# Kernel optimization log

Measured on AMD Instinct MI355X. Metric: run time of the kernel, lower is better.

## Reference

```python
import jax, jax.numpy as jnp
import numpy as np

N, E, B = 100000, 1000000, 64
DIN, DS, H, NG = 128, 1024, 256, 20


def setup_inputs() -> dict:
    key = jax.random.key(0)
    ks = jax.random.split(key, 48)
    lin = lambda k, i, o: (jax.random.normal(k, (i, o), jnp.float32) / np.sqrt(i)).astype(jnp.float32)
    inp = {
        'x': jax.random.normal(ks[0], (N, DIN), jnp.float32),
        'edge_index': jax.random.randint(ks[1], (2, E), 0, N, jnp.int32),
        'batch': jnp.sort(jax.random.randint(ks[2], (N,), 0, B, jnp.int32)),
        'static_features': jax.random.normal(ks[3], (B, DS), jnp.float32),
        'temporal_feats': jax.random.normal(ks[4], (B, 5), jnp.float32),
        'type_idx': jax.random.randint(ks[5], (B,), 0, 10, jnp.int32),
        'type_emb': jax.random.normal(ks[6], (10, H), jnp.float32),
        # static encoder
        'Ws1': lin(ks[7], DS, H), 'bs1': jnp.zeros(H), 'Ws2': lin(ks[8], H, H), 'bs2': jnp.zeros(H),
        # 3 GCN convs
        'Wc1': lin(ks[9], DIN, H), 'bc1': jnp.zeros(H),
        'Wc2': lin(ks[10], H, H), 'bc2': jnp.zeros(H),
        'Wc3': lin(ks[11], H, H), 'bc3': jnp.zeros(H),
        # residual dim_match linears
        'Wd1': lin(ks[12], DIN, H), 'bd1': jnp.zeros(H),
        'Wd2': lin(ks[13], H, H), 'bd2': jnp.zeros(H),
        'Wd3': lin(ks[14], H, H), 'bd3': jnp.zeros(H),
        # temporal MLP (5 -> H//2 -> H)
        'Wt1': lin(ks[15], 5, H // 2), 'bt1': jnp.zeros(H // 2),
        'Wt2': lin(ks[16], H // 2, H), 'bt2': jnp.zeros(H),
        # pattern detector
        'Wp1': lin(ks[17], H, H // 2), 'bp1': jnp.zeros(H // 2),
        'Wp2': lin(ks[18], H // 2, H), 'bp2': jnp.zeros(H),
        # fusion (5H -> 2H -> H)
        'Wf1': lin(ks[19], 5 * H, 2 * H), 'bf1': jnp.zeros(2 * H),
        'Wf2': lin(ks[20], 2 * H, H), 'bf2': jnp.zeros(H),
        # heads
        'Wg': lin(ks[21], H, NG), 'bg': jnp.zeros(NG),
        'Wtp': lin(ks[22], H, 1), 'btp': jnp.zeros(1),
    }
    return inp


def reference(x, edge_index, batch, static_features, temporal_feats, type_idx, type_emb,
              Ws1, bs1, Ws2, bs2,
              Wc1, bc1, Wc2, bc2, Wc3, bc3,
              Wd1, bd1, Wd2, bd2, Wd3, bd3,
              Wt1, bt1, Wt2, bt2,
              Wp1, bp1, Wp2, bp2,
              Wf1, bf1, Wf2, bf2,
              Wg, bg, Wtp, btp):
    n = x.shape[0]
    b = static_features.shape[0]
    src, dst = edge_index[0], edge_index[1]
    # GCN symmetric norm with self-loops: deg = 1 + in-degree
    deg = 1.0 + jax.ops.segment_sum(jnp.ones(src.shape[0], x.dtype), dst, num_segments=n)
    dinv = deg ** -0.5
    ew = dinv[src] * dinv[dst]  # [E] edge norm weights

    def gcn(h_in, W, bias):
        h = h_in @ W  # [n, H]
        agg = jax.ops.segment_sum(h[src] * ew[:, None], dst, num_segments=n)
        return agg + h / deg[:, None] + bias  # neighbor agg + self-loop + bias

    # 3 GCN layers with residual dim_match (dropout is identity at inference)
    x1 = jax.nn.relu(gcn(x, Wc1, bc1)) + (x @ Wd1 + bd1)
    x2 = jax.nn.relu(gcn(x1, Wc2, bc2)) + (x1 @ Wd2 + bd2)
    x3 = jax.nn.relu(gcn(x2, Wc3, bc3)) + (x2 @ Wd3 + bd3)

    pat = jax.nn.relu(jax.nn.relu(x3 @ Wp1 + bp1) @ Wp2 + bp2)

    counts = jnp.maximum(jax.ops.segment_sum(jnp.ones(n, x.dtype), batch, num_segments=b), 1.0)
    graph_embed = jax.ops.segment_sum(x3, batch, num_segments=b) / counts[:, None]
    pattern_embed = jax.ops.segment_sum(pat, batch, num_segments=b) / counts[:, None]

    static_embed = jax.nn.relu(static_features @ Ws1 + bs1) @ Ws2 + bs2
    temporal_embed = jax.nn.relu(temporal_feats @ Wt1 + bt1) @ Wt2 + bt2
    type_embed = type_emb[type_idx]

    combined = jnp.concatenate([graph_embed, static_embed, temporal_embed, type_embed, pattern_embed], axis=1)
    fused = jax.nn.relu(combined @ Wf1 + bf1) @ Wf2 + bf2
    group_logits = fused @ Wg + bg
    time_pred = fused @ Wtp + btp
    return fused, group_logits, time_pred
```

## Files before the change

kernel.cpp:

```cpp
#include <hip/hip_runtime.h>

#define H 256
#define LDK 40

typedef __attribute__((ext_vector_type(8))) short bf16x8;
typedef __attribute__((ext_vector_type(4))) float f32x4;

__device__ __forceinline__ float b2f(ushort h) {
    return __uint_as_float(((unsigned)h) << 16);
}
__device__ __forceinline__ ushort f2bf(float f) {
    unsigned u = __float_as_uint(f);
    unsigned r = (u + 0x7FFF + ((u >> 16) & 1)) >> 16;
    return (ushort)r;
}

__global__ __launch_bounds__(256) void k_zero_i(int* p, int n) {
    int i = blockIdx.x * 256 + threadIdx.x;
    if (i < n) p[i] = 0;
}

__global__ __launch_bounds__(256) void k_zero_f(float* p, int n) {
    int i = blockIdx.x * 256 + threadIdx.x;
    if (i < n) p[i] = 0.f;
}

__global__ __launch_bounds__(256) void k_count_deg_i(const int* __restrict__ dst, int* cnt, int E) {
    int i = blockIdx.x * 256 + threadIdx.x;
    if (i < E) atomicAdd(&cnt[dst[i]], 1);
}

__global__ __launch_bounds__(256) void k_scan1(const int* __restrict__ cnt, int* __restrict__ partial,
                                               int* __restrict__ bsums, int N) {
    __shared__ int s[256];
    int t = threadIdx.x;
    int idx = blockIdx.x * 256 + t;
    int v = idx < N ? cnt[idx] : 0;
    s[t] = v;
    __syncthreads();
    for (int off = 1; off < 256; off <<= 1) {
        int add = (t >= off) ? s[t - off] : 0;
        __syncthreads();
        s[t] += add;
        __syncthreads();
    }
    if (idx < N) partial[idx] = s[t];
    if (t == 255) bsums[blockIdx.x] = s[t];
}

__global__ __launch_bounds__(1024) void k_scan2(int* bsums, int nb) {
    __shared__ int s[1024];
    int t = threadIdx.x;
    s[t] = (t < nb) ? bsums[t] : 0;
    __syncthreads();
    for (int off = 1; off < 1024; off <<= 1) {
        int add = (t >= off) ? s[t - off] : 0;
        __syncthreads();
        s[t] += add;
        __syncthreads();
    }
    if (t < nb) bsums[t] = s[t];
}

__global__ __launch_bounds__(256) void k_scan3(const int* __restrict__ partial, const int* __restrict__ bsums,
                                               int* __restrict__ rowptr, int N) {
    int idx = blockIdx.x * 256 + threadIdx.x;
    if (idx < N) {
        int off = blockIdx.x > 0 ? bsums[blockIdx.x - 1] : 0;
        rowptr[idx + 1] = partial[idx] + off;
        if (idx == 0) rowptr[0] = 0;
    }
}

__global__ __launch_bounds__(256) void k_finish_deg_i(const int* __restrict__ cnt,
                                                      float* __restrict__ dinv,
                                                      float* __restrict__ selfw, int N) {
    int i = blockIdx.x * 256 + threadIdx.x;
    if (i < N) {
        float d = 1.0f + (float)cnt[i];
        dinv[i] = rsqrtf(d);
        selfw[i] = 1.0f / d;
    }
}

__global__ __launch_bounds__(256) void k_scatter(const int* __restrict__ src, const int* __restrict__ dst,
                                                 const float* __restrict__ dinv, const int* __restrict__ rowptr,
                                                 int* __restrict__ fill, int* __restrict__ esrc,
                                                 float* __restrict__ ewt, int E) {
    int e = blockIdx.x * 256 + threadIdx.x;
    if (e >= E) return;
    int s = src[e], d = dst[e];
    int pos = rowptr[d] + atomicAdd(&fill[d], 1);
    esrc[pos] = s;
    ewt[pos] = dinv[s] * dinv[d];
}

__global__ __launch_bounds__(256) void k_cvt(const float* __restrict__ in, ushort* __restrict__ out, long n) {
    long i = (long)blockIdx.x * 256 + threadIdx.x;
    if (i < n) out[i] = f2bf(in[i]);
}

__global__ __launch_bounds__(256) void k_tcvt(const float* __restrict__ W, ushort* __restrict__ Wt,
                                              int K, int M) {
    int idx = blockIdx.x * 256 + threadIdx.x;
    if (idx >= K * M) return;
    int k = idx / M, m = idx - k * M;
    Wt[(size_t)m * K + k] = f2bf(W[idx]);
}

__global__ __launch_bounds__(256) void k_gather_b4(const ushort* __restrict__ xin, const int* __restrict__ rowptr,
                                                   const int* __restrict__ esrc, const float* __restrict__ ewt,
                                                   const float* __restrict__ selfw, ushort* __restrict__ p,
                                                   int N, int SX, int SP) {
    int node = blockIdx.x * 4 + (threadIdx.x >> 6);
    if (node >= N) return;
    int c = (threadIdx.x & 63) << 2;
    ushort4 h = *(const ushort4*)(xin + (size_t)node * SX + c);
    float sw = selfw[node];
    float a0 = b2f(h.x) * sw, a1 = b2f(h.y) * sw, a2 = b2f(h.z) * sw, a3 = b2f(h.w) * sw;
    int j = rowptr[node], r1 = rowptr[node + 1];
    for (; j + 3 < r1; j += 4) {
        int s0 = esrc[j], s1 = esrc[j + 1], s2 = esrc[j + 2], s3 = esrc[j + 3];
        float w0 = ewt[j], w1 = ewt[j + 1], w2 = ewt[j + 2], w3 = ewt[j + 3];
        ushort4 v0 = *(const ushort4*)(xin + (size_t)s0 * SX + c);
        ushort4 v1 = *(const ushort4*)(xin + (size_t)s1 * SX + c);
        ushort4 v2 = *(const ushort4*)(xin + (size_t)s2 * SX + c);
        ushort4 v3 = *(const ushort4*)(xin + (size_t)s3 * SX + c);
        a0 += b2f(v0.x) * w0 + b2f(v1.x) * w1 + b2f(v2.x) * w2 + b2f(v3.x) * w3;
        a1 += b2f(v0.y) * w0 + b2f(v1.y) * w1 + b2f(v2.y) * w2 + b2f(v3.y) * w3;
        a2 += b2f(v0.z) * w0 + b2f(v1.z) * w1 + b2f(v2.z) * w2 + b2f(v3.z) * w3;
        a3 += b2f(v0.w) * w0 + b2f(v1.w) * w1 + b2f(v2.w) * w2 + b2f(v3.w) * w3;
    }
    for (; j < r1; ++j) {
        int s0 = esrc[j];
        float w0 = ewt[j];
        ushort4 v0 = *(const ushort4*)(xin + (size_t)s0 * SX + c);
        a0 += b2f(v0.x) * w0; a1 += b2f(v0.y) * w0; a2 += b2f(v0.z) * w0; a3 += b2f(v0.w) * w0;
    }
    ushort4 o;
    o.x = f2bf(a0); o.y = f2bf(a1); o.z = f2bf(a2); o.w = f2bf(a3);
    *(ushort4*)(p + (size_t)node * SP + c) = o;
}

__global__ __launch_bounds__(256) void k_gather_b2(const ushort* __restrict__ xin, const int* __restrict__ rowptr,
                                                   const int* __restrict__ esrc, const float* __restrict__ ewt,
                                                   const float* __restrict__ selfw, ushort* __restrict__ p,
                                                   int N, int SX, int SP) {
    int node = blockIdx.x * 4 + (threadIdx.x >> 6);
    if (node >= N) return;
    int c = (threadIdx.x & 63) << 1;
    ushort2 h = *(const ushort2*)(xin + (size_t)node * SX + c);
    float sw = selfw[node];
    float a0 = b2f(h.x) * sw, a1 = b2f(h.y) * sw;
    int j = rowptr[node], r1 = rowptr[node + 1];
    for (; j + 3 < r1; j += 4) {
        int s0 = esrc[j], s1 = esrc[j + 1], s2 = esrc[j + 2], s3 = esrc[j + 3];
        float w0 = ewt[j], w1 = ewt[j + 1], w2 = ewt[j + 2], w3 = ewt[j + 3];
        ushort2 v0 = *(const ushort2*)(xin + (size_t)s0 * SX + c);
        ushort2 v1 = *(const ushort2*)(xin + (size_t)s1 * SX + c);
        ushort2 v2 = *(const ushort2*)(xin + (size_t)s2 * SX + c);
        ushort2 v3 = *(const ushort2*)(xin + (size_t)s3 * SX + c);
        a0 += b2f(v0.x) * w0 + b2f(v1.x) * w1 + b2f(v2.x) * w2 + b2f(v3.x) * w3;
        a1 += b2f(v0.y) * w0 + b2f(v1.y) * w1 + b2f(v2.y) * w2 + b2f(v3.y) * w3;
    }
    for (; j < r1; ++j) {
        int s0 = esrc[j];
        float w0 = ewt[j];
        ushort2 v0 = *(const ushort2*)(xin + (size_t)s0 * SX + c);
        a0 += b2f(v0.x) * w0; a1 += b2f(v0.y) * w0;
    }
    ushort2 o;
    o.x = f2bf(a0); o.y = f2bf(a1);
    *(ushort2*)(p + (size_t)node * SP + c) = o;
}

__global__ __launch_bounds__(256, 2) void k_fused_mfma(
    const ushort* __restrict__ Pm, const ushort* __restrict__ X,
    const ushort* __restrict__ Wct, const ushort* __restrict__ Wdt,
    const float* __restrict__ bc, const float* __restrict__ bd,
    ushort* __restrict__ Out, int N, int K, int SP, int SX) {
    __shared__ short Ps[64 * LDK];
    __shared__ short Xs[64 * LDK];
    __shared__ short Wcs[256 * LDK];
    __shared__ short Wds[256 * LDK];
    const int tid = threadIdx.x;
    const int wave = tid >> 6, lane = tid & 63;
    const int row0 = blockIdx.x * 64;

    f32x4 accC[4][4], accD[4][4];
#pragma unroll
    for (int i = 0; i < 4; ++i)
#pragma unroll
        for (int j = 0; j < 4; ++j) { accC[i][j] = (f32x4)0.f; accD[i][j] = (f32x4)0.f; }

    const int sr = tid >> 2, sc = (tid & 3) * 8;
    int grow = row0 + sr; if (grow > N - 1) grow = N - 1;
    const int m = lane & 15, kh = (lane >> 4) * 8;

    for (int k0 = 0; k0 < K; k0 += 32) {
        *(uint4*)&Ps[sr * LDK + sc] = *(const uint4*)(Pm + (size_t)grow * SP + k0 + sc);
        *(uint4*)&Xs[sr * LDK + sc] = *(const uint4*)(X + (size_t)grow * SX + k0 + sc);
#pragma unroll
        for (int p = 0; p < 4; ++p) {
            int col = p * 64 + (tid >> 2);
            *(uint4*)&Wcs[col * LDK + sc] = *(const uint4*)(Wct + (size_t)col * K + k0 + sc);
            *(uint4*)&Wds[col * LDK + sc] = *(const uint4*)(Wdt + (size_t)col * K + k0 + sc);
        }
        __syncthreads();
        bf16x8 aP[4], aX[4], bC[4], bD[4];
#pragma unroll
        for (int i = 0; i < 4; ++i) {
            aP[i] = *(bf16x8*)&Ps[(16 * i + m) * LDK + kh];
            aX[i] = *(bf16x8*)&Xs[(16 * i + m) * LDK + kh];
        }
#pragma unroll
        for (int j = 0; j < 4; ++j) {
            int c = wave * 64 + 16 * j + m;
            bC[j] = *(bf16x8*)&Wcs[c * LDK + kh];
            bD[j] = *(bf16x8*)&Wds[c * LDK + kh];
        }
#pragma unroll
        for (int i = 0; i < 4; ++i)
#pragma unroll
            for (int j = 0; j < 4; ++j) {
                accC[i][j] = __builtin_amdgcn_mfma_f32_16x16x32_bf16(aP[i], bC[j], accC[i][j], 0, 0, 0);
                accD[i][j] = __builtin_amdgcn_mfma_f32_16x16x32_bf16(aX[i], bD[j], accD[i][j], 0, 0, 0);
            }
        __syncthreads();
    }

    const int rq = (lane >> 4) * 4;
#pragma unroll
    for (int j = 0; j < 4; ++j) {
        int col = wave * 64 + 16 * j + m;
        float bcv = bc[col], bdv = bd[col];
#pragma unroll
        for (int i = 0; i < 4; ++i)
#pragma unroll
            for (int g = 0; g < 4; ++g) {
                int row = row0 + 16 * i + rq + g;
                if (row < N) {
                    float v = fmaxf(accC[i][j][g] + bcv, 0.f) + accD[i][j][g] + bdv;
                    Out[(size_t)row * 256 + col] = f2bf(v);
                }
            }
    }
}

__global__ __launch_bounds__(256, 2) void k_gemm_mfma(
    const ushort* __restrict__ A, const ushort* __restrict__ Wt, const float* __restrict__ bias,
    ushort* __restrict__ Out, int N, int K, int M, int SA, int dorelu) {
    __shared__ short As[128 * LDK];
    __shared__ short Wls[256 * LDK];
    const int tid = threadIdx.x;
    const int wave = tid >> 6, lane = tid & 63;
    const int MW = M >> 6;
    const int R = 16384 / M;
    const int row0 = blockIdx.x * R;
    const int row_off = (wave / MW) * 64, col_off = (wave % MW) * 64;

    f32x4 acc[4][4];
#pragma unroll
    for (int i = 0; i < 4; ++i)
#pragma unroll
        for (int j = 0; j < 4; ++j) acc[i][j] = (f32x4)0.f;

    const int m = lane & 15, kh = (lane >> 4) * 8, sc = (tid & 3) * 8;

    for (int k0 = 0; k0 < K; k0 += 32) {
        for (int c = tid; c < R * 4; c += 256) {
            int r = c >> 2, ck = (c & 3) * 8;
            int gr = row0 + r; if (gr > N - 1) gr = N - 1;
            *(uint4*)&As[r * LDK + ck] = *(const uint4*)(A + (size_t)gr * SA + k0 + ck);
        }
        for (int p = 0; p < MW; ++p) {
            int col = p * 64 + (tid >> 2);
            *(uint4*)&Wls[col * LDK + sc] = *(const uint4*)(Wt + (size_t)col * K + k0 + sc);
        }
        __syncthreads();
        bf16x8 af[4], bf[4];
#pragma unroll
        for (int i = 0; i < 4; ++i) af[i] = *(bf16x8*)&As[(row_off + 16 * i + m) * LDK + kh];
#pragma unroll
        for (int j = 0; j < 4; ++j) bf[j] = *(bf16x8*)&Wls[(col_off + 16 * j + m) * LDK + kh];
#pragma unroll
        for (int i = 0; i < 4; ++i)
#pragma unroll
            for (int j = 0; j < 4; ++j)
                acc[i][j] = __builtin_amdgcn_mfma_f32_16x16x32_bf16(af[i], bf[j], acc[i][j], 0, 0, 0);
        __syncthreads();
    }

    const int rq = (lane >> 4) * 4;
#pragma unroll
    for (int j = 0; j < 4; ++j) {
        int col = col_off + 16 * j + m;
        float bv = bias[col];
#pragma unroll
        for (int i = 0; i < 4; ++i)
#pragma unroll
            for (int g = 0; g < 4; ++g) {
                int row = row0 + row_off + 16 * i + rq + g;
                if (row < N) {
                    float v = acc[i][j][g] + bv;
                    if (dorelu) v = fmaxf(v, 0.f);
                    Out[(size_t)row * M + col] = f2bf(v);
                }
            }
    }
}

__global__ __launch_bounds__(256, 2) void k_pat2_pool(
    const ushort* __restrict__ A, const ushort* __restrict__ Wt, const float* __restrict__ bias,
    const int* __restrict__ batch, float* __restrict__ pesum, int N, int K, int SA) {
    __shared__ short As[64 * LDK];
    __shared__ short Wls[256 * LDK];
    __shared__ int sbatch[64];
    const int tid = threadIdx.x;
    const int wave = tid >> 6, lane = tid & 63;
    const int row0 = blockIdx.x * 64;
    const int col_off = wave * 64;

    f32x4 acc[4][4];
#pragma unroll
    for (int i = 0; i < 4; ++i)
#pragma unroll
        for (int j = 0; j < 4; ++j) acc[i][j] = (f32x4)0.f;

    const int m = lane & 15, kh = (lane >> 4) * 8, sc = (tid & 3) * 8;
    if (tid < 64) {
        int r = row0 + tid;
        sbatch[tid] = batch[r < N ? r : (N - 1)];
    }

    for (int k0 = 0; k0 < K; k0 += 32) {
        {
            int r = tid >> 2, ck = (tid & 3) * 8;
            int gr = row0 + r; if (gr > N - 1) gr = N - 1;
            *(uint4*)&As[r * LDK + ck] = *(const uint4*)(A + (size_t)gr * SA + k0 + ck);
        }
#pragma unroll
        for (int p = 0; p < 4; ++p) {
            int col = p * 64 + (tid >> 2);
            *(uint4*)&Wls[col * LDK + sc] = *(const uint4*)(Wt + (size_t)col * K + k0 + sc);
        }
        __syncthreads();
        bf16x8 af[4], bf[4];
#pragma unroll
        for (int i = 0; i < 4; ++i) af[i] = *(bf16x8*)&As[(16 * i + m) * LDK + kh];
#pragma unroll
        for (int j = 0; j < 4; ++j) bf[j] = *(bf16x8*)&Wls[(col_off + 16 * j + m) * LDK + kh];
#pragma unroll
        for (int i = 0; i < 4; ++i)
#pragma unroll
            for (int j = 0; j < 4; ++j)
                acc[i][j] = __builtin_amdgcn_mfma_f32_16x16x32_bf16(af[i], bf[j], acc[i][j], 0, 0, 0);
        __syncthreads();
    }

    const int rq = (lane >> 4) * 4;
    const int g0 = sbatch[0];
    const int g1 = sbatch[63];
    for (int g = g0; g <= g1; ++g) {
#pragma unroll
        for (int j = 0; j < 4; ++j) {
            float bv = bias[col_off + 16 * j + m];
            float s = 0.f;
#pragma unroll
            for (int i = 0; i < 4; ++i)
#pragma unroll
                for (int q = 0; q < 4; ++q) {
                    int rl = 16 * i + rq + q;
                    bool ok = (sbatch[rl] == g) && (row0 + rl < N);
                    float v = fmaxf(acc[i][j][q] + bv, 0.f);
                    s += ok ? v : 0.f;
                }
            s += __shfl_down(s, 32, 64);
            s += __shfl_down(s, 16, 64);
            if (lane < 16) atomicAdd(&pesum[(size_t)g * 256 + col_off + 16 * j + lane], s);
        }
    }
}

__global__ void k_ranges(const int* __restrict__ batch, int N, int B, int* __restrict__ start,
                         float* __restrict__ countsf) {
    int b = threadIdx.x;
    if (b <= B) {
        int lo = 0, hi = N;
        while (lo < hi) {
            int mid = (lo + hi) >> 1;
            if (batch[mid] < b) lo = mid + 1; else hi = mid;
        }
        start[b] = lo;
    }
    __syncthreads();
    if (b < B) {
        int cnt = start[b + 1] - start[b];
        countsf[b] = (float)(cnt > 0 ? cnt : 1);
    }
}

#define POOLS 16
__global__ __launch_bounds__(256) void k_pool2(const ushort* __restrict__ M_, const int* __restrict__ start,
                                               float* __restrict__ outsum) {
    int b = blockIdx.x;
    int s = blockIdx.y;
    int wave = threadIdx.x >> 6, lane = threadIdx.x & 63;
    int r0 = start[b], r1 = start[b + 1];
    int stripe = s * 4 + wave;
    float a0 = 0.f, a1 = 0.f, a2 = 0.f, a3 = 0.f;
    for (int r = r0 + stripe; r < r1; r += POOLS * 4) {
        ushort4 v = *(const ushort4*)(M_ + (size_t)r * 256 + lane * 4);
        a0 += b2f(v.x); a1 += b2f(v.y); a2 += b2f(v.z); a3 += b2f(v.w);
    }
    __shared__ float red[4][256];
    *(float4*)&red[wave][lane * 4] = make_float4(a0, a1, a2, a3);
    __syncthreads();
    int col = threadIdx.x;
    float t = red[0][col] + red[1][col] + red[2][col] + red[3][col];
    if (t != 0.f) atomicAdd(&outsum[(size_t)b * 256 + col], t);
}

__global__ __launch_bounds__(256) void k_pool_fin(float* __restrict__ ge, float* __restrict__ pe,
                                                  const float* __restrict__ countsf) {
    int b = blockIdx.x, t = threadIdx.x;
    float inv = 1.0f / countsf[b];
    ge[(size_t)b * 256 + t] *= inv;
    pe[(size_t)b * 256 + t] *= inv;
}

__global__ __launch_bounds__(256) void k_dense(const float* __restrict__ vin, int vs,
                                               const float* __restrict__ W, const float* __restrict__ bias,
                                               float* __restrict__ out, int os, int oo,
                                               int K, int M, int relu) {
    const int b = blockIdx.y;
    const int wave = threadIdx.x >> 6, lane = threadIdx.x & 63;
    const int c = blockIdx.x * 64 + lane;
    const float* vrow = vin + (size_t)b * vs;
    float acc = 0.f;
    int k = wave;
    for (; k + 28 < K; k += 32) {
#pragma unroll
        for (int u = 0; u < 8; ++u)
            acc += vrow[k + 4 * u] * W[(size_t)(k + 4 * u) * M + c];
    }
    for (; k < K; k += 4)
        acc += vrow[k] * W[(size_t)k * M + c];
    __shared__ float red[4][64];
    red[wave][lane] = acc;
    __syncthreads();
    if (wave == 0) {
        float s = red[0][lane] + red[1][lane] + red[2][lane] + red[3][lane] + bias[c];
        if (relu) s = fmaxf(s, 0.f);
        out[(size_t)b * os + oo + c] = s;
    }
}

__global__ __launch_bounds__(256) void k_comb(const float* __restrict__ ge, const float* __restrict__ pe,
                                              const float* __restrict__ temb, const int* __restrict__ tidx,
                                              float* __restrict__ comb) {
    int b = blockIdx.x, t = threadIdx.x;
    float* o = comb + (size_t)b * 1280;
    o[t] = ge[(size_t)b * 256 + t];
    o[768 + t] = temb[(size_t)tidx[b] * 256 + t];
    o[1024 + t] = pe[(size_t)b * 256 + t];
}

__global__ __launch_bounds__(256) void k_heads_small(const float* __restrict__ fused,
                                                     const float* __restrict__ Wg, const float* __restrict__ bg,
                                                     const float* __restrict__ Wtp, const float* __restrict__ btp,
                                                     float* __restrict__ out_logits, float* __restrict__ out_tp,
                                                     int NG) {
    __shared__ float lf[256];
    int b = blockIdx.x, tid = threadIdx.x;
    int wave = tid >> 6, lane = tid & 63;
    lf[tid] = fused[(size_t)b * 256 + tid];
    __syncthreads();
    for (int c = wave; c < NG; c += 4) {
        float s = 0.f;
#pragma unroll
        for (int k = lane; k < 256; k += 64) s += lf[k] * Wg[(size_t)k * NG + c];
#pragma unroll
        for (int off = 32; off > 0; off >>= 1) s += __shfl_down(s, off, 64);
        if (lane == 0) out_logits[(size_t)b * NG + c] = s + bg[c];
    }
    if (wave == 0) {
        float s = 0.f;
#pragma unroll
        for (int k = lane; k < 256; k += 64) s += lf[k] * Wtp[k];
#pragma unroll
        for (int off = 32; off > 0; off >>= 1) s += __shfl_down(s, off, 64);
        if (lane == 0) out_tp[b] = s + btp[0];
    }
}

extern "C" void kernel_launch(void* const* d_in, const int* in_sizes, int n_in,
                              void* d_out, int out_size, void* d_ws, size_t ws_size,
                              hipStream_t stream) {
    const float* x   = (const float*)d_in[0];
    const int* ei    = (const int*)d_in[1];
    const int* batch = (const int*)d_in[2];
    const float* sf  = (const float*)d_in[3];
    const float* tf  = (const float*)d_in[4];
    const int* tidx  = (const int*)d_in[5];
    const float* temb = (const float*)d_in[6];
    const float *Ws1 = (const float*)d_in[7],  *bs1 = (const float*)d_in[8];
    const float *Ws2 = (const float*)d_in[9],  *bs2 = (const float*)d_in[10];
    const float *Wc1 = (const float*)d_in[11], *bc1 = (const float*)d_in[12];
    const float *Wc2 = (const float*)d_in[13], *bc2 = (const float*)d_in[14];
    const float *Wc3 = (const float*)d_in[15], *bc3 = (const float*)d_in[16];
    const float *Wd1 = (const float*)d_in[17], *bd1 = (const float*)d_in[18];
    const float *Wd2 = (const float*)d_in[19], *bd2 = (const float*)d_in[20];
    const float *Wd3 = (const float*)d_in[21], *bd3 = (const float*)d_in[22];
    const float *Wt1 = (const float*)d_in[23], *bt1 = (const float*)d_in[24];
    const float *Wt2 = (const float*)d_in[25], *bt2 = (const float*)d_in[26];
    const float *Wp1 = (const float*)d_in[27], *bp1 = (const float*)d_in[28];
    const float *Wp2 = (const float*)d_in[29], *bp2 = (const float*)d_in[30];
    const float *Wf1 = (const float*)d_in[31], *bf1 = (const float*)d_in[32];
    const float *Wf2 = (const float*)d_in[33], *bf2 = (const float*)d_in[34];
    const float *Wg  = (const float*)d_in[35], *bg  = (const float*)d_in[36];
    const float *Wtp = (const float*)d_in[37], *btp = (const float*)d_in[38];

    const int N = in_sizes[2];
    const int E = in_sizes[1] / 2;
    const int B = in_sizes[5];
    const int DS = in_sizes[3] / B;
    const int NG = in_sizes[36];
    const int* src = ei;
    const int* dst = ei + E;

    char* w = (char*)d_ws;
    ushort* A   = (ushort*)w;              w += (size_t)N * 256 * 2;
    ushort* Bb  = (ushort*)w;              w += (size_t)N * 256 * 2;
    ushort* xh  = (ushort*)w;              w += (size_t)N * 128 * 2;
    ushort* Wc1t = (ushort*)w;             w += 128 * 256 * 2;
    ushort* Wd1t = (ushort*)w;             w += 128 * 256 * 2;
    ushort* Wc2t = (ushort*)w;             w += 256 * 256 * 2;
    ushort* Wd2t = (ushort*)w;             w += 256 * 256 * 2;
    ushort* Wc3t = (ushort*)w;             w += 256 * 256 * 2;
    ushort* Wd3t = (ushort*)w;             w += 256 * 256 * 2;
    ushort* Wp1t = (ushort*)w;             w += 256 * 128 * 2;
    ushort* Wp2t = (ushort*)w;             w += 128 * 256 * 2;
    int* esrc   = (int*)w;                 w += (size_t)E * 4;
    float* ewt  = (float*)w;               w += (size_t)E * 4;
    int* cnt    = (int*)w;                 w += (size_t)N * 4;
    int* part   = (int*)w;                 w += (size_t)N * 4;
    int* rowptr = (int*)w;                 w += (size_t)(N + 1) * 4;
    int* fill   = (int*)w;                 w += (size_t)N * 4;
    int* bsums  = (int*)w;                 w += 1024 * 4;
    float* dinv = (float*)w;               w += (size_t)N * 4;
    float* selfw = (float*)w;              w += (size_t)N * 4;
    int* startp = (int*)w;                 w += (B + 1) * 4;
    float* countsf = (float*)w;            w += B * 4;
    float* ge = (float*)w;                 w += B * 256 * 4;
    float* pe = (float*)w;                 w += B * 256 * 4;
    float* s1buf = (float*)w;              w += B * 256 * 4;
    float* t1buf = (float*)w;              w += B * 128 * 4;
    float* comb = (float*)w;               w += B * 1280 * 4;
    float* fh = (float*)w;                 w += B * 512 * 4;

    float* out_fused = (float*)d_out;
    float* out_logits = out_fused + (size_t)B * H;
    float* out_tp = out_logits + (size_t)B * NG;

    dim3 blk(256);
    const int nbN = (N + 255) / 256;
    const int nbE = (E + 255) / 256;

    k_zero_i<<<dim3(nbN), blk, 0, stream>>>(cnt, N);
    k_zero_i<<<dim3(nbN), blk, 0, stream>>>(fill, N);
    k_count_deg_i<<<dim3(nbE), blk, 0, stream>>>(dst, cnt, E);
    k_scan1<<<dim3(nbN), blk, 0, stream>>>(cnt, part, bsums, N);
    k_scan2<<<dim3(1), dim3(1024), 0, stream>>>(bsums, nbN);
    k_scan3<<<dim3(nbN), blk, 0, stream>>>(part, bsums, rowptr, N);
    k_finish_deg_i<<<dim3(nbN), blk, 0, stream>>>(cnt, dinv, selfw, N);
    k_scatter<<<dim3(nbE), blk, 0, stream>>>(src, dst, dinv, rowptr, fill, esrc, ewt, E);

    {
        long nx = (long)N * 128;
        k_cvt<<<dim3((unsigned)((nx + 255) / 256)), blk, 0, stream>>>(x, xh, nx);
        k_tcvt<<<dim3((128 * 256 + 255) / 256), blk, 0, stream>>>(Wc1, Wc1t, 128, 256);
        k_tcvt<<<dim3((128 * 256 + 255) / 256), blk, 0, stream>>>(Wd1, Wd1t, 128, 256);
        k_tcvt<<<dim3((256 * 256 + 255) / 256), blk, 0, stream>>>(Wc2, Wc2t, 256, 256);
        k_tcvt<<<dim3((256 * 256 + 255) / 256), blk, 0, stream>>>(Wd2, Wd2t, 256, 256);
        k_tcvt<<<dim3((256 * 256 + 255) / 256), blk, 0, stream>>>(Wc3, Wc3t, 256, 256);
        k_tcvt<<<dim3((256 * 256 + 255) / 256), blk, 0, stream>>>(Wd3, Wd3t, 256, 256);
        k_tcvt<<<dim3((256 * 128 + 255) / 256), blk, 0, stream>>>(Wp1, Wp1t, 256, 128);
        k_tcvt<<<dim3((128 * 256 + 255) / 256), blk, 0, stream>>>(Wp2, Wp2t, 128, 256);
        k_ranges<<<dim3(1), dim3(128), 0, stream>>>(batch, N, B, startp, countsf);
        k_zero_f<<<dim3((2 * B * 256 + 255) / 256), blk, 0, stream>>>(ge, 2 * B * 256);
    }

    const int ngb = (N + 3) / 4;
    const int nfb = (N + 63) / 64;

    k_dense<<<dim3(4, B), blk, 0, stream>>>(sf, DS, Ws1, bs1, s1buf, 256, 0, DS, 256, 1);
    k_dense<<<dim3(4, B), blk, 0, stream>>>(s1buf, 256, Ws2, bs2, comb, 1280, 256, 256, 256, 0);
    k_dense<<<dim3(2, B), blk, 0, stream>>>(tf, 5, Wt1, bt1, t1buf, 128, 0, 5, 128, 1);
    k_dense<<<dim3(4, B), blk, 0, stream>>>(t1buf, 128, Wt2, bt2, comb, 1280, 512, 128, 256, 0);

    k_gather_b2<<<dim3(ngb), blk, 0, stream>>>(xh, rowptr, esrc, ewt, selfw, A, N, 128, 128);
    k_fused_mfma<<<dim3(nfb), blk, 0, stream>>>(A, xh, Wc1t, Wd1t, bc1, bd1, Bb, N, 128, 128, 128);
    k_gather_b4<<<dim3(ngb), blk, 0, stream>>>(Bb, rowptr, esrc, ewt, selfw, A, N, 256, 256);
    k_fused_mfma<<<dim3(nfb), blk, 0, stream>>>(A, Bb, Wc2t, Wd2t, bc2, bd2, A, N, 256, 256, 256);
    k_gather_b4<<<dim3(ngb), blk, 0, stream>>>(A, rowptr, esrc, ewt, selfw, Bb, N, 256, 256);
    k_fused_mfma<<<dim3(nfb), blk, 0, stream>>>(Bb, A, Wc3t, Wd3t, bc3, bd3, Bb, N, 256, 256, 256);

    k_pool2<<<dim3(B, POOLS), blk, 0, stream>>>(Bb, startp, ge);
    k_gemm_mfma<<<dim3((N + 127) / 128), blk, 0, stream>>>(Bb, Wp1t, bp1, A, N, 256, 128, 256, 1);
    k_pat2_pool<<<dim3(nfb), blk, 0, stream>>>(A, Wp2t, bp2, batch, pe, N, 128, 128);
    k_pool_fin<<<dim3(B), blk, 0, stream>>>(ge, pe, countsf);

    k_comb<<<dim3(B), blk, 0, stream>>>(ge, pe, temb, tidx, comb);
    k_dense<<<dim3(8, B), blk, 0, stream>>>(comb, 1280, Wf1, bf1, fh, 512, 0, 1280, 512, 1);
    k_dense<<<dim3(4, B), blk, 0, stream>>>(fh, 512, Wf2, bf2, out_fused, 256, 0, 512, 256, 0);
    k_heads_small<<<dim3(B), blk, 0, stream>>>(out_fused, Wg, bg, Wtp, btp, out_logits, out_tp, NG);
}
```

Baseline: 897.7 us.

## Merge small prep kernels and enlarge fused MFMA tile to 128 rows

Collapses many tiny launches into single kernels: the two zeroing kernels become one, the degree finish folds into scan3, x conversion and the eight weight transposes become one k_prep launch, and pool finalisation merges with the combine step. The fused GCN MFMA kernel moves to 512 threads covering a 128-row tile, so each weight tile staged in shared memory serves twice as many rows. This cuts launch overhead and weight reloads, but the larger shared-memory footprint and block size may lower occupancy. The staging load for the 128-row P/X tile relies on sr covering 128 rows with 512 threads, which it does (tid>>2).

```diff
diff --git a/kernel.cpp b/kernel.cpp
--- a/kernel.cpp
+++ b/kernel.cpp
@@ -15,9 +15,9 @@
     return (ushort)r;
 }
 
-__global__ __launch_bounds__(256) void k_zero_i(int* p, int n) {
+__global__ __launch_bounds__(256) void k_zero2_i(int* p, int* q, int n) {
     int i = blockIdx.x * 256 + threadIdx.x;
-    if (i < n) p[i] = 0;
+    if (i < n) { p[i] = 0; q[i] = 0; }
 }
 
 __global__ __launch_bounds__(256) void k_zero_f(float* p, int n) {
@@ -63,23 +63,17 @@
 }
 
 __global__ __launch_bounds__(256) void k_scan3(const int* __restrict__ partial, const int* __restrict__ bsums,
-                                               int* __restrict__ rowptr, int N) {
+                                               const int* __restrict__ cnt,
+                                               int* __restrict__ rowptr, float* __restrict__ dinv,
+                                               float* __restrict__ selfw, int N) {
     int idx = blockIdx.x * 256 + threadIdx.x;
     if (idx < N) {
         int off = blockIdx.x > 0 ? bsums[blockIdx.x - 1] : 0;
         rowptr[idx + 1] = partial[idx] + off;
         if (idx == 0) rowptr[0] = 0;
-    }
-}
-
-__global__ __launch_bounds__(256) void k_finish_deg_i(const int* __restrict__ cnt,
-                                                      float* __restrict__ dinv,
-                                                      float* __restrict__ selfw, int N) {
-    int i = blockIdx.x * 256 + threadIdx.x;
-    if (i < N) {
-        float d = 1.0f + (float)cnt[i];
-        dinv[i] = rsqrtf(d);
-        selfw[i] = 1.0f / d;
+        float d = 1.0f + (float)cnt[idx];
+        dinv[idx] = rsqrtf(d);
+        selfw[idx] = 1.0f / d;
     }
 }
 
@@ -95,17 +89,37 @@
     ewt[pos] = dinv[s] * dinv[d];
 }
 
-__global__ __launch_bounds__(256) void k_cvt(const float* __restrict__ in, ushort* __restrict__ out, long n) {
+__device__ __forceinline__ void tcvt_one(long i, const float* __restrict__ W, ushort* __restrict__ Wt,
+                                         int K, int M) {
+    int k = (int)(i / M), m = (int)(i - (long)k * M);
+    Wt[(size_t)m * K + k] = f2bf(W[(size_t)k * M + m]);
+}
+
+__global__ __launch_bounds__(256) void k_prep(
+    const float* __restrict__ x, ushort* __restrict__ xh, long nx, int DIN,
+    const float* __restrict__ Wc1, ushort* Wc1t, const float* __restrict__ Wd1, ushort* Wd1t,
+    const float* __restrict__ Wc2, ushort* Wc2t, const float* __restrict__ Wd2, ushort* Wd2t,
+    const float* __restrict__ Wc3, ushort* Wc3t, const float* __restrict__ Wd3, ushort* Wd3t,
+    const float* __restrict__ Wp1, ushort* Wp1t, const float* __restrict__ Wp2, ushort* Wp2t) {
     long i = (long)blockIdx.x * 256 + threadIdx.x;
-    if (i < n) out[i] = f2bf(in[i]);
-}
-
-__global__ __launch_bounds__(256) void k_tcvt(const float* __restrict__ W, ushort* __restrict__ Wt,
-                                              int K, int M) {
-    int idx = blockIdx.x * 256 + threadIdx.x;
-    if (idx >= K * M) return;
-    int k = idx / M, m = idx - k * M;
-    Wt[(size_t)m * K + k] = f2bf(W[idx]);
+    if (i < nx) { xh[i] = f2bf(x[i]); return; }
+    i -= nx;
+    long n1 = (long)DIN * 256;
+    if (i < n1) { tcvt_one(i, Wc1, Wc1t, DIN, 256); return; }
+    i -= n1;
+    if (i < n1) { tcvt_one(i, Wd1, Wd1t, DIN, 256); return; }
+    i -= n1;
+    if (i < 65536) { tcvt_one(i, Wc2, Wc2t, 256, 256); return; }
+    i -= 65536;
+    if (i < 65536) { tcvt_one(i, Wd2, Wd2t, 256, 256); return; }
+    i -= 65536;
+    if (i < 65536) { tcvt_one(i, Wc3, Wc3t, 256, 256); return; }
+    i -= 65536;
+    if (i < 65536) { tcvt_one(i, Wd3, Wd3t, 256, 256); return; }
+    i -= 65536;
+    if (i < 32768) { tcvt_one(i, Wp1, Wp1t, 256, 128); return; }
+    i -= 32768;
+    if (i < 32768) { tcvt_one(i, Wp2, Wp2t, 128, 256); return; }
 }
 
 __global__ __launch_bounds__(256) void k_gather_b4(const ushort* __restrict__ xin, const int* __restrict__ rowptr,
@@ -174,18 +188,19 @@
     *(ushort2*)(p + (size_t)node * SP + c) = o;
 }
 
-__global__ __launch_bounds__(256, 2) void k_fused_mfma(
+__global__ __launch_bounds__(512, 4) void k_fused_mfma(
     const ushort* __restrict__ Pm, const ushort* __restrict__ X,
     const ushort* __restrict__ Wct, const ushort* __restrict__ Wdt,
     const float* __restrict__ bc, const float* __restrict__ bd,
     ushort* __restrict__ Out, int N, int K, int SP, int SX) {
-    __shared__ short Ps[64 * LDK];
-    __shared__ short Xs[64 * LDK];
+    __shared__ short Ps[128 * LDK];
+    __shared__ short Xs[128 * LDK];
     __shared__ short Wcs[256 * LDK];
     __shared__ short Wds[256 * LDK];
     const int tid = threadIdx.x;
     const int wave = tid >> 6, lane = tid & 63;
-    const int row0 = blockIdx.x * 64;
+    const int rh = wave >> 2, cq = wave & 3;
+    const int row0 = blockIdx.x * 128;
 
     f32x4 accC[4][4], accD[4][4];
 #pragma unroll
@@ -201,8 +216,8 @@
         *(uint4*)&Ps[sr * LDK + sc] = *(const uint4*)(Pm + (size_t)grow * SP + k0 + sc);
         *(uint4*)&Xs[sr * LDK + sc] = *(const uint4*)(X + (size_t)grow * SX + k0 + sc);
 #pragma unroll
-        for (int p = 0; p < 4; ++p) {
-            int col = p * 64 + (tid >> 2);
+        for (int p = 0; p < 2; ++p) {
+            int col = p * 128 + (tid >> 2);
             *(uint4*)&Wcs[col * LDK + sc] = *(const uint4*)(Wct + (size_t)col * K + k0 + sc);
             *(uint4*)&Wds[col * LDK + sc] = *(const uint4*)(Wdt + (size_t)col * K + k0 + sc);
         }
@@ -210,12 +225,12 @@
         bf16x8 aP[4], aX[4], bC[4], bD[4];
 #pragma unroll
         for (int i = 0; i < 4; ++i) {
-            aP[i] = *(bf16x8*)&Ps[(16 * i + m) * LDK + kh];
-            aX[i] = *(bf16x8*)&Xs[(16 * i + m) * LDK + kh];
+            aP[i] = *(bf16x8*)&Ps[(rh * 64 + 16 * i + m) * LDK + kh];
+            aX[i] = *(bf16x8*)&Xs[(rh * 64 + 16 * i + m) * LDK + kh];
         }
 #pragma unroll
         for (int j = 0; j < 4; ++j) {
-            int c = wave * 64 + 16 * j + m;
+            int c = cq * 64 + 16 * j + m;
             bC[j] = *(bf16x8*)&Wcs[c * LDK + kh];
             bD[j] = *(bf16x8*)&Wds[c * LDK + kh];
         }
@@ -232,13 +247,13 @@
     const int rq = (lane >> 4) * 4;
 #pragma unroll
     for (int j = 0; j < 4; ++j) {
-        int col = wave * 64 + 16 * j + m;
+        int col = cq * 64 + 16 * j + m;
         float bcv = bc[col], bdv = bd[col];
 #pragma unroll
         for (int i = 0; i < 4; ++i)
 #pragma unroll
             for (int g = 0; g < 4; ++g) {
-                int row = row0 + 16 * i + rq + g;
+                int row = row0 + rh * 64 + 16 * i + rq + g;
                 if (row < N) {
                     float v = fmaxf(accC[i][j][g] + bcv, 0.f) + accD[i][j][g] + bdv;
                     Out[(size_t)row * 256 + col] = f2bf(v);
@@ -421,12 +436,16 @@
     if (t != 0.f) atomicAdd(&outsum[(size_t)b * 256 + col], t);
 }
 
-__global__ __launch_bounds__(256) void k_pool_fin(float* __restrict__ ge, float* __restrict__ pe,
-                                                  const float* __restrict__ countsf) {
+__global__ __launch_bounds__(256) void k_fin_comb(const float* __restrict__ gesum, const float* __restrict__ pesum,
+                                                  const float* __restrict__ countsf,
+                                                  const float* __restrict__ temb, const int* __restrict__ tidx,
+                                                  float* __restrict__ comb) {
     int b = blockIdx.x, t = threadIdx.x;
     float inv = 1.0f / countsf[b];
-    ge[(size_t)b * 256 + t] *= inv;
-    pe[(size_t)b * 256 + t] *= inv;
+    float* o = comb + (size_t)b * 1280;
+    o[t] = gesum[(size_t)b * 256 + t] * inv;
+    o[768 + t] = temb[(size_t)tidx[b] * 256 + t];
+    o[1024 + t] = pesum[(size_t)b * 256 + t] * inv;
 }
 
 __global__ __launch_bounds__(256) void k_dense(const float* __restrict__ vin, int vs,
@@ -454,16 +473,6 @@
         if (relu) s = fmaxf(s, 0.f);
         out[(size_t)b * os + oo + c] = s;
     }
-}
-
-__global__ __launch_bounds__(256) void k_comb(const float* __restrict__ ge, const float* __restrict__ pe,
-                                              const float* __restrict__ temb, const int* __restrict__ tidx,
-                                              float* __restrict__ comb) {
-    int b = blockIdx.x, t = threadIdx.x;
-    float* o = comb + (size_t)b * 1280;
-    o[t] = ge[(size_t)b * 256 + t];
-    o[768 + t] = temb[(size_t)tidx[b] * 256 + t];
-    o[1024 + t] = pe[(size_t)b * 256 + t];
 }
 
 __global__ __launch_bounds__(256) void k_heads_small(const float* __restrict__ fused,
@@ -524,6 +533,7 @@
     const int N = in_sizes[2];
     const int E = in_sizes[1] / 2;
     const int B = in_sizes[5];
+    const int DIN = in_sizes[0] / N;
     const int DS = in_sizes[3] / B;
     const int NG = in_sizes[36];
     const int* src = ei;
@@ -567,32 +577,25 @@
     const int nbN = (N + 255) / 256;
     const int nbE = (E + 255) / 256;
 
-    k_zero_i<<<dim3(nbN), blk, 0, stream>>>(cnt, N);
-    k_zero_i<<<dim3(nbN), blk, 0, stream>>>(fill, N);
+    k_zero2_i<<<dim3(nbN), blk, 0, stream>>>(cnt, fill, N);
     k_count_deg_i<<<dim3(nbE), blk, 0, stream>>>(dst, cnt, E);
     k_scan1<<<dim3(nbN), blk, 0, stream>>>(cnt, part, bsums, N);
     k_scan2<<<dim3(1), dim3(1024), 0, stream>>>(bsums, nbN);
-    k_scan3<<<dim3(nbN), blk, 0, stream>>>(part, bsums, rowptr, N);
-    k_finish_deg_i<<<dim3(nbN), blk, 0, stream>>>(cnt, dinv, selfw, N);
+    k_scan3<<<dim3(nbN), blk, 0, stream>>>(part, bsums, cnt, rowptr, dinv, selfw, N);
     k_scatter<<<dim3(nbE), blk, 0, stream>>>(src, dst, dinv, rowptr, fill, esrc, ewt, E);
 
     {
-        long nx = (long)N * 128;
-        k_cvt<<<dim3((unsigned)((nx + 255) / 256)), blk, 0, stream>>>(x, xh, nx);
-        k_tcvt<<<dim3((128 * 256 + 255) / 256), blk, 0, stream>>>(Wc1, Wc1t, 128, 256);
-        k_tcvt<<<dim3((128 * 256 + 255) / 256), blk, 0, stream>>>(Wd1, Wd1t, 128, 256);
-        k_tcvt<<<dim3((256 * 256 + 255) / 256), blk, 0, stream>>>(Wc2, Wc2t, 256, 256);
-        k_tcvt<<<dim3((256 * 256 + 255) / 256), blk, 0, stream>>>(Wd2, Wd2t, 256, 256);
-        k_tcvt<<<dim3((256 * 256 + 255) / 256), blk, 0, stream>>>(Wc3, Wc3t, 256, 256);
-        k_tcvt<<<dim3((256 * 256 + 255) / 256), blk, 0, stream>>>(Wd3, Wd3t, 256, 256);
-        k_tcvt<<<dim3((256 * 128 + 255) / 256), blk, 0, stream>>>(Wp1, Wp1t, 256, 128);
-        k_tcvt<<<dim3((128 * 256 + 255) / 256), blk, 0, stream>>>(Wp2, Wp2t, 128, 256);
+        long nx = (long)N * DIN;
+        long tot = nx + 2L * DIN * 256 + 4L * 65536 + 2L * 32768;
+        k_prep<<<dim3((unsigned)((tot + 255) / 256)), blk, 0, stream>>>(
+            x, xh, nx, DIN, Wc1, Wc1t, Wd1, Wd1t, Wc2, Wc2t, Wd2, Wd2t,
+            Wc3, Wc3t, Wd3, Wd3t, Wp1, Wp1t, Wp2, Wp2t);
         k_ranges<<<dim3(1), dim3(128), 0, stream>>>(batch, N, B, startp, countsf);
         k_zero_f<<<dim3((2 * B * 256 + 255) / 256), blk, 0, stream>>>(ge, 2 * B * 256);
     }
 
     const int ngb = (N + 3) / 4;
-    const int nfb = (N + 63) / 64;
+    const int nfb = (N + 127) / 128;
 
     k_dense<<<dim3(4, B), blk, 0, stream>>>(sf, DS, Ws1, bs1, s1buf, 256, 0, DS, 256, 1);
     k_dense<<<dim3(4, B), blk, 0, stream>>>(s1buf, 256, Ws2, bs2, comb, 1280, 256, 256, 256, 0);
@@ -600,18 +603,17 @@
     k_dense<<<dim3(4, B), blk, 0, stream>>>(t1buf, 128, Wt2, bt2, comb, 1280, 512, 128, 256, 0);
 
     k_gather_b2<<<dim3(ngb), blk, 0, stream>>>(xh, rowptr, esrc, ewt, selfw, A, N, 128, 128);
-    k_fused_mfma<<<dim3(nfb), blk, 0, stream>>>(A, xh, Wc1t, Wd1t, bc1, bd1, Bb, N, 128, 128, 128);
+    k_fused_mfma<<<dim3(nfb), dim3(512), 0, stream>>>(A, xh, Wc1t, Wd1t, bc1, bd1, Bb, N, 128, 128, 128);
     k_gather_b4<<<dim3(ngb), blk, 0, stream>>>(Bb, rowptr, esrc, ewt, selfw, A, N, 256, 256);
-    k_fused_mfma<<<dim3(nfb), blk, 0, stream>>>(A, Bb, Wc2t, Wd2t, bc2, bd2, A, N, 256, 256, 256);
+    k_fused_mfma<<<dim3(nfb), dim3(512), 0, stream>>>(A, Bb, Wc2t, Wd2t, bc2, bd2, A, N, 256, 256, 256);
     k_gather_b4<<<dim3(ngb), blk, 0, stream>>>(A, rowptr, esrc, ewt, selfw, Bb, N, 256, 256);
-    k_fused_mfma<<<dim3(nfb), blk, 0, stream>>>(Bb, A, Wc3t, Wd3t, bc3, bd3, Bb, N, 256, 256, 256);
+    k_fused_mfma<<<dim3(nfb), dim3(512), 0, stream>>>(Bb, A, Wc3t, Wd3t, bc3, bd3, Bb, N, 256, 256, 256);
 
     k_pool2<<<dim3(B, POOLS), blk, 0, stream>>>(Bb, startp, ge);
     k_gemm_mfma<<<dim3((N + 127) / 128), blk, 0, stream>>>(Bb, Wp1t, bp1, A, N, 256, 128, 256, 1);
-    k_pat2_pool<<<dim3(nfb), blk, 0, stream>>>(A, Wp2t, bp2, batch, pe, N, 128, 128);
-    k_pool_fin<<<dim3(B), blk, 0, stream>>>(ge, pe, countsf);
-
-    k_comb<<<dim3(B), blk, 0, stream>>>(ge, pe, temb, tidx, comb);
+    k_pat2_pool<<<dim3((N + 63) / 64), blk, 0, stream>>>(A, Wp2t, bp2, batch, pe, N, 128, 128);
+    k_fin_comb<<<dim3(B), blk, 0, stream>>>(ge, pe, countsf, temb, tidx, comb);
+
     k_dense<<<dim3(8, B), blk, 0, stream>>>(comb, 1280, Wf1, bf1, fh, 512, 0, 1280, 512, 1);
     k_dense<<<dim3(4, B), blk, 0, stream>>>(fh, 512, Wf2, bf2, out_fused, 256, 0, 512, 256, 0);
     k_heads_small<<<dim3(B), blk, 0, stream>>>(out_fused, Wg, bg, Wtp, btp, out_logits, out_tp, NG);
```

Result: slower. 1.417 ms (+57.9%).
